# Optimization experiments

Hardware: AMD Instinct MI355X
Metric: run time of the kernel (lower is better)

The kernel has to match this reference:

```python
import jax, jax.numpy as jnp
import numpy as np

N = 50000      # nodes
E = 1600000    # edges (before self loops)
F_IN = 1433    # input features (Cora)
H1, C1 = 8, 8  # layer1: heads, out channels per head
C2 = 7         # layer2: classes (heads=1, concat=False)
SLOPE = 0.2    # PyG GATConv default negative_slope


def _gat_layer(x, src, dst, W, a_src, a_dst, b, heads, out_ch, concat):
    """PyG-style GATConv (eval mode, self loops already in src/dst)."""
    n = x.shape[0]
    h = (x @ W).reshape(n, heads, out_ch)                 # [N,H,C]
    alpha_s = jnp.einsum('nhc,hc->nh', h, a_src)          # [N,H]
    alpha_d = jnp.einsum('nhc,hc->nh', h, a_dst)          # [N,H]
    e = jax.nn.leaky_relu(alpha_s[src] + alpha_d[dst], SLOPE)  # [E,H]
    # segment softmax over incoming edges per destination node
    m = jax.ops.segment_max(e, dst, num_segments=n)       # [N,H]
    ex = jnp.exp(e - m[dst])
    denom = jax.ops.segment_sum(ex, dst, num_segments=n)  # [N,H]
    alpha = ex / (denom[dst] + 1e-16)                     # [E,H]
    out = jax.ops.segment_sum(h[src] * alpha[..., None], dst, num_segments=n)  # [N,H,C]
    out = out.reshape(n, heads * out_ch) if concat else out.mean(axis=1)
    return out + b


def setup_inputs() -> dict:
    key = jax.random.key(0)
    ks = jax.random.split(key, 10)
    x = jax.random.normal(ks[0], (N, F_IN), jnp.float32)
    edge_index = jax.random.randint(ks[1], (2, E), 0, N, jnp.int32)
    s = 0.1
    return {
        'x': x,
        'edge_index': edge_index,
        'W1': jax.random.normal(ks[2], (F_IN, H1 * C1), jnp.float32) * s,
        'att_src1': jax.random.normal(ks[3], (H1, C1), jnp.float32) * s,
        'att_dst1': jax.random.normal(ks[4], (H1, C1), jnp.float32) * s,
        'b1': jnp.zeros((H1 * C1,), jnp.float32),
        'W2': jax.random.normal(ks[5], (H1 * C1, C2), jnp.float32) * s,
        'att_src2': jax.random.normal(ks[6], (1, C2), jnp.float32) * s,
        'att_dst2': jax.random.normal(ks[7], (1, C2), jnp.float32) * s,
        'b2': jnp.zeros((C2,), jnp.float32),
    }


def reference(x, edge_index, W1, att_src1, att_dst1, b1, W2, att_src2, att_dst2, b2):
    loop = jnp.arange(N, dtype=edge_index.dtype)
    src = jnp.concatenate([edge_index[0], loop])   # add_self_loops=True
    dst = jnp.concatenate([edge_index[1], loop])
    h = _gat_layer(x, src, dst, W1, att_src1, att_dst1, b1, H1, C1, True)   # [N,64]
    h = jax.nn.elu(h)
    out = _gat_layer(h, src, dst, W2, att_src2, att_dst2, b2, 1, C2, False)  # [N,7]
    return jax.nn.log_softmax(out, axis=1)
```

## Files before the change

kernel.cpp:

```cpp
#include <hip/hip_runtime.h>
#include <hip/hip_bf16.h>

static constexpr int NN      = 50000;
static constexpr int FIN     = 1433;
static constexpr int KPAD    = 1440;
static constexpr int NB_SCAN = (NN + 255) / 256;
static constexpr int L1B     = NN / 4;

typedef __bf16 bf16x8 __attribute__((ext_vector_type(8)));
typedef float  f32x4  __attribute__((ext_vector_type(4)));

__device__ __forceinline__ float leaky02(float v){ return v >= 0.f ? v : 0.2f * v; }
__device__ __forceinline__ float bflo(unsigned u){ return __uint_as_float(u << 16); }
__device__ __forceinline__ float bfhi(unsigned u){ return __uint_as_float(u & 0xffff0000u); }

__device__ __forceinline__ void gld_lds4(const float* g, float* l){
    __builtin_amdgcn_global_load_lds(
        (const __attribute__((address_space(1))) unsigned int*)g,
        (__attribute__((address_space(3))) unsigned int*)l, 4, 0, 0);
}

__global__ __launch_bounds__(256) void k_prep(const float* __restrict__ W1,
                                              __bf16* __restrict__ w1h, __bf16* __restrict__ w1l,
                                              int* __restrict__ deg){
    int bid = blockIdx.x;
    if (bid < 64){
        int c = bid;
        for (int k = threadIdx.x; k < KPAD; k += 256){
            float v = (k < FIN) ? W1[(size_t)k * 64 + c] : 0.f;
            __bf16 hi = (__bf16)v;
            w1h[(size_t)c * KPAD + k] = hi;
            w1l[(size_t)c * KPAD + k] = (__bf16)(v - (float)hi);
        }
    } else {
        int i = (bid - 64) * 256 + threadIdx.x;
        if (i < NN) deg[i] = 0;
    }
}

__global__ __launch_bounds__(256) void k_rank(const int* __restrict__ dst, int* __restrict__ deg,
                                              int* __restrict__ rank, int E){
    int base = blockIdx.x * 1024 + threadIdx.x;
    int d[4]; bool v[4];
    #pragma unroll
    for (int i = 0; i < 4; ++i){
        int e = base + i * 256;
        v[i] = e < E;
        d[i] = v[i] ? dst[e] : 0;
    }
    int r[4];
    #pragma unroll
    for (int i = 0; i < 4; ++i)
        if (v[i]) r[i] = atomicAdd(&deg[d[i]], 1);
    #pragma unroll
    for (int i = 0; i < 4; ++i)
        if (v[i]) rank[base + i * 256] = r[i];
}

__global__ __launch_bounds__(256) void k_scan1(const int* __restrict__ deg, int* __restrict__ bsum){
    __shared__ int red[256];
    int i = blockIdx.x * 256 + threadIdx.x;
    red[threadIdx.x] = (i < NN) ? deg[i] : 0;
    __syncthreads();
    for (int off = 128; off > 0; off >>= 1){
        if (threadIdx.x < off) red[threadIdx.x] += red[threadIdx.x + off];
        __syncthreads();
    }
    if (threadIdx.x == 0) bsum[blockIdx.x] = red[0];
}

__global__ __launch_bounds__(256) void k_scan3(const int* __restrict__ deg, const int* __restrict__ bsum,
                                               int* __restrict__ row_off){
    __shared__ int s[256];
    int t = threadIdx.x;
    int i = blockIdx.x * 256 + t;
    s[t] = (t < blockIdx.x) ? bsum[t] : 0;
    __syncthreads();
    for (int off = 128; off > 0; off >>= 1){
        if (t < off) s[t] += s[t + off];
        __syncthreads();
    }
    int bofs = s[0];
    __syncthreads();
    int d = (i < NN) ? deg[i] : 0;
    s[t] = d;
    __syncthreads();
    for (int off = 1; off < 256; off <<= 1){
        int v = s[t];
        int a = (t >= off) ? s[t - off] : 0;
        __syncthreads();
        s[t] = v + a;
        __syncthreads();
    }
    int excl = s[t] - d + bofs;
    if (i < NN){
        row_off[i] = excl;
        if (i == NN - 1) row_off[NN] = excl + d;
    }
}

__global__ __launch_bounds__(256) void k_scatter(const int* __restrict__ src, const int* __restrict__ dst,
                                                 const int* __restrict__ rank, const int* __restrict__ row_off,
                                                 int* __restrict__ csr, int E){
    int base = blockIdx.x * 1024 + threadIdx.x;
    int d[4], r[4], sv[4]; bool v[4];
    #pragma unroll
    for (int i = 0; i < 4; ++i){
        int e = base + i * 256;
        v[i] = e < E;
        if (v[i]){ d[i] = dst[e]; r[i] = rank[e]; sv[i] = src[e]; }
    }
    int ro[4];
    #pragma unroll
    for (int i = 0; i < 4; ++i)
        if (v[i]) ro[i] = row_off[d[i]];
    #pragma unroll
    for (int i = 0; i < 4; ++i)
        if (v[i]) csr[ro[i] + r[i]] = sv[i];
}

__global__ __launch_bounds__(256, 4) void k_gemm1(const float* __restrict__ x,
    const __bf16* __restrict__ w1h, const __bf16* __restrict__ w1l,
    const float* __restrict__ a_s, const float* __restrict__ a_d,
    __bf16* __restrict__ Hb, __bf16* __restrict__ asad)
{
    __shared__ float  As[64 * 68];
    __shared__ __bf16 AH[64 * 72];
    __shared__ __bf16 AL[64 * 72];
    const int tid  = threadIdx.x;
    const int w    = tid >> 6;
    const int lane = tid & 63;
    const int lr   = lane & 15;
    const int lk   = lane >> 4;
    const int rbase = blockIdx.x * 64;
    const int cr = tid >> 2;
    const int cg = (tid & 3) * 16;

    unsigned rowoff[16];
    #pragma unroll
    for (int i = 0; i < 16; ++i){
        int rg = rbase + w * 16 + i; if (rg >= NN) rg = NN - 1;
        rowoff[i] = (unsigned)rg * (unsigned)FIN + (unsigned)lane;
    }

    const __bf16* bh_p = w1h + (size_t)(w * 16 + lr) * KPAD + lk * 8;
    const __bf16* bl_p = w1l + (size_t)(w * 16 + lr) * KPAD + lk * 8;

    f32x4 acc[4] = {{0,0,0,0},{0,0,0,0},{0,0,0,0},{0,0,0,0}};

    #pragma unroll
    for (int i = 0; i < 16; ++i)
        gld_lds4(x + rowoff[i], &As[(w * 16 + i) * 68]);
    __syncthreads();

    for (int kb = 0; kb < 22; ++kb){
        {
            const float* rp = &As[cr * 68 + cg];
            f32x4 v[4];
            #pragma unroll
            for (int j = 0; j < 4; ++j) v[j] = *(const f32x4*)(rp + j * 4);
            bf16x8 hv0, hv1, lv0, lv1;
            #pragma unroll
            for (int j = 0; j < 2; ++j){
                #pragma unroll
                for (int e = 0; e < 4; ++e){
                    float a0 = v[2 * j][e], a1 = v[2 * j + 1][e];
                    __bf16 h0 = (__bf16)a0, h1 = (__bf16)a1;
                    if (j == 0){ hv0[e] = h0; hv0[e + 4] = h1;
                                 lv0[e] = (__bf16)(a0 - (float)h0);
                                 lv0[e + 4] = (__bf16)(a1 - (float)h1); }
                    else       { hv1[e] = h0; hv1[e + 4] = h1;
                                 lv1[e] = (__bf16)(a0 - (float)h0);
                                 lv1[e + 4] = (__bf16)(a1 - (float)h1); }
                }
            }
            *(bf16x8*)&AH[cr * 72 + cg]     = hv0;
            *(bf16x8*)&AH[cr * 72 + cg + 8] = hv1;
            *(bf16x8*)&AL[cr * 72 + cg]     = lv0;
            *(bf16x8*)&AL[cr * 72 + cg + 8] = lv1;
        }
        __syncthreads();

        if (kb < 21){
            const float* gsrc = x + (kb + 1) * 64;
            #pragma unroll
            for (int i = 0; i < 16; ++i)
                gld_lds4(gsrc + rowoff[i], &As[(w * 16 + i) * 68]);
        }

        const int kA = kb * 64;
        bf16x8 bh0 = *(const bf16x8*)(bh_p + kA);
        bf16x8 bl0 = *(const bf16x8*)(bl_p + kA);
        bf16x8 bh1 = *(const bf16x8*)(bh_p + kA + 32);
        bf16x8 bl1 = *(const bf16x8*)(bl_p + kA + 32);
        #pragma unroll
        for (int ks = 0; ks < 2; ++ks){
            bf16x8 bh = ks ? bh1 : bh0;
            bf16x8 bl = ks ? bl1 : bl0;
            #pragma unroll
            for (int t = 0; t < 4; ++t){
                const int ao = (t * 16 + lr) * 72 + ks * 32 + lk * 8;
                bf16x8 ah = *(const bf16x8*)&AH[ao];
                bf16x8 al = *(const bf16x8*)&AL[ao];
                acc[t] = __builtin_amdgcn_mfma_f32_16x16x32_bf16(ah, bh, acc[t], 0, 0, 0);
                acc[t] = __builtin_amdgcn_mfma_f32_16x16x32_bf16(al, bh, acc[t], 0, 0, 0);
                acc[t] = __builtin_amdgcn_mfma_f32_16x16x32_bf16(ah, bl, acc[t], 0, 0, 0);
            }
        }
        __syncthreads();
    }

    {
        bf16x8 bh = *(const bf16x8*)(bh_p + 1408);
        bf16x8 bl = *(const bf16x8*)(bl_p + 1408);
        #pragma unroll
        for (int t = 0; t < 4; ++t){
            int rg = rbase + t * 16 + lr; if (rg >= NN) rg = NN - 1;
            const float* xr = x + (size_t)rg * FIN;
            bf16x8 ah, al;
            #pragma unroll
            for (int e = 0; e < 8; ++e){
                int k = 1408 + lk * 8 + e;
                float v = (k < FIN) ? xr[k] : 0.f;
                __bf16 h = (__bf16)v;
                ah[e] = h; al[e] = (__bf16)(v - (float)h);
            }
            acc[t] = __builtin_amdgcn_mfma_f32_16x16x32_bf16(ah, bh, acc[t], 0, 0, 0);
            acc[t] = __builtin_amdgcn_mfma_f32_16x16x32_bf16(al, bh, acc[t], 0, 0, 0);
            acc[t] = __builtin_amdgcn_mfma_f32_16x16x32_bf16(ah, bl, acc[t], 0, 0, 0);
        }
    }

    __syncthreads();
    const int col = w * 16 + lr;
    #pragma unroll
    for (int t = 0; t < 4; ++t){
        #pragma unroll
        for (int r = 0; r < 4; ++r){
            int rib = t * 16 + lk * 4 + r;
            float v = acc[t][r];
            As[rib * 68 + col] = v;
            int row = rbase + rib;
            if (row < NN) Hb[(size_t)row * 64 + col] = (__bf16)v;
        }
    }
    __syncthreads();
    #pragma unroll
    for (int it = 0; it < 2; ++it){
        int task = tid + it * 256;
        int row  = task >> 3;
        int hh   = task & 7;
        int grow = rbase + row;
        if (grow < NN){
            const float* hr = &As[row * 68 + hh * 8];
            float s = 0.f, dd = 0.f;
            #pragma unroll
            for (int c = 0; c < 8; ++c){
                float v = hr[c];
                s  = fmaf(v, a_s[hh * 8 + c], s);
                dd = fmaf(v, a_d[hh * 8 + c], dd);
            }
            asad[(size_t)grow * 16 + hh]     = (__bf16)s;
            asad[(size_t)grow * 16 + 8 + hh] = (__bf16)dd;
        }
    }
}

__global__ __launch_bounds__(256, 8) void k_layer1(const __bf16* __restrict__ asad,
    const __bf16* __restrict__ Hb, const int* __restrict__ row_off, const int* __restrict__ csr,
    const float* __restrict__ b1, float* __restrict__ x2)
{
    const int d  = blockIdx.x * 4 + (threadIdx.x >> 6);
    const int l  = threadIdx.x & 63;
    const int e8 = l >> 3;
    const int c8 = l & 7;
    const int c0 = c8 * 8;
    const float adv = (float)asad[(size_t)d * 16 + 8 + c8];

    float den = 0.f;
    float a[8] = {0.f,0.f,0.f,0.f,0.f,0.f,0.f,0.f};
    if (e8 == 0){
        float as_d = (float)asad[(size_t)d * 16 + c8];
        float p0 = __expf(leaky02(as_d + adv) - 20.f);
        uint4 hw = *(const uint4*)&Hb[(size_t)d * 64 + c0];
        den = p0;
        a[0] = p0 * bflo(hw.x); a[1] = p0 * bfhi(hw.x);
        a[2] = p0 * bflo(hw.y); a[3] = p0 * bfhi(hw.y);
        a[4] = p0 * bflo(hw.z); a[5] = p0 * bfhi(hw.z);
        a[6] = p0 * bflo(hw.w); a[7] = p0 * bfhi(hw.w);
    }

    const int beg = row_off[d], end = row_off[d + 1];
    const int nb = (end - beg + 7) >> 3;
    int csrv = 0;
    if (nb > 0){
        int idx = beg + c8; if (idx >= end) idx = end - 1;
        csrv = __builtin_nontemporal_load(csr + idx);
    }
    for (int b = 0; b < nb; ++b){
        const int base = beg + b * 8;
        int ncsr = 0;
        if (b + 1 < nb){
            int idx = base + 8 + c8; if (idx >= end) idx = end - 1;
            ncsr = __builtin_nontemporal_load(csr + idx);
        }
        int s = __shfl(csrv, e8, 8);
        const bool val = (base + e8) < end;
        uint4 hw = make_uint4(0u,0u,0u,0u); float av = 0.f;
        if (val){
            hw = *(const uint4*)&Hb[(size_t)s * 64 + c0];
            av = (float)asad[(size_t)s * 16 + c8];
        }
        if (val){
            float p = __expf(leaky02(av + adv) - 20.f);
            den += p;
            a[0] = fmaf(p, bflo(hw.x), a[0]); a[1] = fmaf(p, bfhi(hw.x), a[1]);
            a[2] = fmaf(p, bflo(hw.y), a[2]); a[3] = fmaf(p, bfhi(hw.y), a[3]);
            a[4] = fmaf(p, bflo(hw.z), a[4]); a[5] = fmaf(p, bfhi(hw.z), a[5]);
            a[6] = fmaf(p, bflo(hw.w), a[6]); a[7] = fmaf(p, bfhi(hw.w), a[7]);
        }
        csrv = ncsr;
    }

    #pragma unroll
    for (int m = 8; m <= 32; m <<= 1){
        den += __shfl_xor(den, m, 64);
        #pragma unroll
        for (int j = 0; j < 8; ++j) a[j] += __shfl_xor(a[j], m, 64);
    }

    if (e8 == 0){
        float inv = 1.f / den;
        float o[8];
        #pragma unroll
        for (int j = 0; j < 8; ++j){
            float v = a[j] * inv + b1[c0 + j];
            o[j] = (v > 0.f) ? v : (__expf(v) - 1.f);
        }
        float4 o0 = make_float4(o[0], o[1], o[2], o[3]);
        float4 o1 = make_float4(o[4], o[5], o[6], o[7]);
        float* xp = &x2[(size_t)d * 64 + c0];
        *(float4*)xp       = o0;
        *(float4*)(xp + 4) = o1;
    }
}

__global__ __launch_bounds__(256) void k_gemm2(const float* __restrict__ x2, const float* __restrict__ W2,
    const float* __restrict__ aw_in, const float* __restrict__ dw_in,
    float* __restrict__ h2a, float* __restrict__ ad2)
{
    __shared__ float w2s[448];
    __shared__ float aw[7], dw[7];
    int tid = threadIdx.x;
    for (int i = tid; i < 448; i += 256) w2s[i] = W2[i];
    if (tid < 7){ aw[tid] = aw_in[tid]; dw[tid] = dw_in[tid]; }
    __syncthreads();
    int n = blockIdx.x * 256 + tid;
    if (n >= NN) return;
    const float4* xp = (const float4*)(x2 + (size_t)n * 64);
    float acc[7] = {0.f,0.f,0.f,0.f,0.f,0.f,0.f};
    #pragma unroll
    for (int q = 0; q < 16; ++q){
        float4 v = xp[q];
        float vv[4] = {v.x, v.y, v.z, v.w};
        #pragma unroll
        for (int u = 0; u < 4; ++u){
            int k = q * 4 + u;
            #pragma unroll
            for (int c = 0; c < 7; ++c) acc[c] = fmaf(vv[u], w2s[k * 7 + c], acc[c]);
        }
    }
    float s = 0.f, d = 0.f;
    #pragma unroll
    for (int c = 0; c < 7; ++c){ s = fmaf(acc[c], aw[c], s); d = fmaf(acc[c], dw[c], d); }
    float* hp = h2a + (size_t)n * 8;
    #pragma unroll
    for (int c = 0; c < 7; ++c) hp[c] = acc[c];
    hp[7] = s;
    ad2[n] = d;
}

__global__ __launch_bounds__(256) void k_layer2(const float* __restrict__ ad2,
    const float* __restrict__ h2a, const int* __restrict__ row_off, const int* __restrict__ csr,
    const float* __restrict__ b2, float* __restrict__ out)
{
    int tid  = threadIdx.x;
    int node = blockIdx.x * 32 + (tid >> 3);
    int c    = tid & 7;
    int lane = tid & 63;
    int gb   = lane & ~7;
    if (node >= NN) return;
    float adv   = ad2[node];
    float vself = h2a[(size_t)node * 8 + c];
    float as_n  = __shfl(vself, gb + 7, 64);
    float e0 = leaky02(as_n + adv);
    float p0 = __expf(e0 - 20.f);
    float den = p0;
    float acc = p0 * vself;
    int beg = row_off[node], end = row_off[node + 1];
    for (int base = beg; base < end; base += 16){
        int cnt = end - base; if (cnt > 16) cnt = 16;
        int j1  = 8 + c;
        int cs0 = csr[base + (c  < cnt ? c  : cnt - 1)];
        int cs1 = csr[base + (j1 < cnt ? j1 : cnt - 1)];
        float val[16];
        #pragma unroll
        for (int t = 0; t < 16; ++t){
            if (t < cnt){
                int s = (t < 8) ? __shfl(cs0, gb + t, 64) : __shfl(cs1, gb + t - 8, 64);
                val[t] = h2a[(size_t)s * 8 + c];
            }
        }
        #pragma unroll
        for (int t = 0; t < 16; ++t){
            if (t < cnt){
                float as_s = __shfl(val[t], gb + 7, 64);
                float e = leaky02(as_s + adv);
                float p = __expf(e - 20.f);
                den += p;
                acc  = fmaf(p, val[t], acc);
            }
        }
    }
    float v = (c < 7) ? (acc / den + b2[c]) : -1e30f;
    float m = v;
    m = fmaxf(m, __shfl_xor(m, 1, 64));
    m = fmaxf(m, __shfl_xor(m, 2, 64));
    m = fmaxf(m, __shfl_xor(m, 4, 64));
    float ex = (c < 7) ? __expf(v - m) : 0.f;
    float s7 = ex;
    s7 += __shfl_xor(s7, 1, 64);
    s7 += __shfl_xor(s7, 2, 64);
    s7 += __shfl_xor(s7, 4, 64);
    if (c < 7) out[(size_t)node * 7 + c] = v - m - __logf(s7);
}

extern "C" void kernel_launch(void* const* d_in, const int* in_sizes, int n_in,
                              void* d_out, int out_size, void* d_ws, size_t ws_size,
                              hipStream_t stream)
{
    (void)n_in; (void)out_size; (void)ws_size;
    const float* x      = (const float*)d_in[0];
    const int*   ei     = (const int*)d_in[1];
    const int    E      = in_sizes[1] / 2;
    const float* W1     = (const float*)d_in[2];
    const float* asrc1  = (const float*)d_in[3];
    const float* adst1  = (const float*)d_in[4];
    const float* b1     = (const float*)d_in[5];
    const float* W2     = (const float*)d_in[6];
    const float* asrc2  = (const float*)d_in[7];
    const float* adst2  = (const float*)d_in[8];
    const float* b2     = (const float*)d_in[9];
    float* out = (float*)d_out;

    char* p = (char*)d_ws;
    auto alloc = [&](size_t bytes) -> void* {
        void* r = (void*)p;
        p += (bytes + 255) & ~(size_t)255;
        return r;
    };
    int*    deg     = (int*)alloc((size_t)NN * 4);
    int*    row_off = (int*)alloc((size_t)(NN + 1) * 4);
    int*    rank    = (int*)alloc((size_t)E * 4);
    int*    bsum    = (int*)alloc((size_t)NB_SCAN * 4);
    int*    csr     = (int*)alloc((size_t)E * 4);
    __bf16* w1h     = (__bf16*)alloc((size_t)64 * KPAD * 2);
    __bf16* w1l     = (__bf16*)alloc((size_t)64 * KPAD * 2);
    __bf16* Hb      = (__bf16*)alloc((size_t)NN * 64 * 2);
    __bf16* asad    = (__bf16*)alloc((size_t)NN * 16 * 2);
    float*  x2      = (float*)alloc((size_t)NN * 64 * 4);
    float*  h2a     = (float*)alloc((size_t)NN * 8 * 4);
    float*  ad2     = (float*)alloc((size_t)NN * 4);

    const int* src = ei;
    const int* dst = ei + E;

    k_prep   <<<64 + NB_SCAN, 256, 0, stream>>>(W1, w1h, w1l, deg);
    k_rank   <<<(E + 1023) / 1024, 256, 0, stream>>>(dst, deg, rank, E);
    k_scan1  <<<NB_SCAN, 256, 0, stream>>>(deg, bsum);
    k_scan3  <<<NB_SCAN, 256, 0, stream>>>(deg, bsum, row_off);
    k_scatter<<<(E + 1023) / 1024, 256, 0, stream>>>(src, dst, rank, row_off, csr, E);
    k_gemm1  <<<(NN + 63) / 64, 256, 0, stream>>>(x, w1h, w1l, asrc1, adst1, Hb, asad);
    k_layer1 <<<L1B, 256, 0, stream>>>(asad, Hb, row_off, csr, b1, x2);
    k_gemm2  <<<(NN + 255) / 256, 256, 0, stream>>>(x2, W2, asrc2, adst2, h2a, ad2);
    k_layer2 <<<(NN + 31) / 32, 256, 0, stream>>>(ad2, h2a, row_off, csr, b2, out);
}
```

Before: 298.3 us.

## Recompute attention logits from gathered features and compress layer-2 records to bf16

The per-node attention scores are no longer produced in the first GEMM and stored to a separate array. The layer-1 aggregation now recomputes the source and destination logits from the gathered bf16 feature rows, which removes one random gather per edge and the GEMM epilogue with its LDS round-trip. Layer 2 stores its per-node record (7 features plus source score) as 16-byte bf16 instead of 32-byte fp32. It also switches to one edge per lane with per-lane accumulation and a shuffle reduction, matching the layer-1 pattern. This trades extra FMAs per edge and some bf16 precision in layer 2 for less gather traffic.

```diff
diff --git a/kernel.cpp b/kernel.cpp
--- a/kernel.cpp
+++ b/kernel.cpp
@@ -121,8 +121,7 @@
 
 __global__ __launch_bounds__(256, 4) void k_gemm1(const float* __restrict__ x,
     const __bf16* __restrict__ w1h, const __bf16* __restrict__ w1l,
-    const float* __restrict__ a_s, const float* __restrict__ a_d,
-    __bf16* __restrict__ Hb, __bf16* __restrict__ asad)
+    __bf16* __restrict__ Hb)
 {
     __shared__ float  As[64 * 68];
     __shared__ __bf16 AH[64 * 72];
@@ -231,42 +230,19 @@
         }
     }
 
-    __syncthreads();
     const int col = w * 16 + lr;
     #pragma unroll
     for (int t = 0; t < 4; ++t){
         #pragma unroll
         for (int r = 0; r < 4; ++r){
-            int rib = t * 16 + lk * 4 + r;
-            float v = acc[t][r];
-            As[rib * 68 + col] = v;
-            int row = rbase + rib;
-            if (row < NN) Hb[(size_t)row * 64 + col] = (__bf16)v;
-        }
-    }
-    __syncthreads();
-    #pragma unroll
-    for (int it = 0; it < 2; ++it){
-        int task = tid + it * 256;
-        int row  = task >> 3;
-        int hh   = task & 7;
-        int grow = rbase + row;
-        if (grow < NN){
-            const float* hr = &As[row * 68 + hh * 8];
-            float s = 0.f, dd = 0.f;
-            #pragma unroll
-            for (int c = 0; c < 8; ++c){
-                float v = hr[c];
-                s  = fmaf(v, a_s[hh * 8 + c], s);
-                dd = fmaf(v, a_d[hh * 8 + c], dd);
-            }
-            asad[(size_t)grow * 16 + hh]     = (__bf16)s;
-            asad[(size_t)grow * 16 + 8 + hh] = (__bf16)dd;
-        }
-    }
-}
-
-__global__ __launch_bounds__(256, 8) void k_layer1(const __bf16* __restrict__ asad,
+            int row = rbase + t * 16 + lk * 4 + r;
+            if (row < NN) Hb[(size_t)row * 64 + col] = (__bf16)acc[t][r];
+        }
+    }
+}
+
+__global__ __launch_bounds__(256, 8) void k_layer1(const float* __restrict__ a_s,
+    const float* __restrict__ a_d,
     const __bf16* __restrict__ Hb, const int* __restrict__ row_off, const int* __restrict__ csr,
     const float* __restrict__ b1, float* __restrict__ x2)
 {
@@ -275,19 +251,31 @@
     const int e8 = l >> 3;
     const int c8 = l & 7;
     const int c0 = c8 * 8;
-    const float adv = (float)asad[(size_t)d * 16 + 8 + c8];
+
+    float asw[8], adw[8];
+    #pragma unroll
+    for (int j = 0; j < 8; ++j){ asw[j] = a_s[c0 + j]; adw[j] = a_d[c0 + j]; }
 
     float den = 0.f;
     float a[8] = {0.f,0.f,0.f,0.f,0.f,0.f,0.f,0.f};
-    if (e8 == 0){
-        float as_d = (float)asad[(size_t)d * 16 + c8];
-        float p0 = __expf(leaky02(as_d + adv) - 20.f);
-        uint4 hw = *(const uint4*)&Hb[(size_t)d * 64 + c0];
-        den = p0;
-        a[0] = p0 * bflo(hw.x); a[1] = p0 * bfhi(hw.x);
-        a[2] = p0 * bflo(hw.y); a[3] = p0 * bfhi(hw.y);
-        a[4] = p0 * bflo(hw.z); a[5] = p0 * bfhi(hw.z);
-        a[6] = p0 * bflo(hw.w); a[7] = p0 * bfhi(hw.w);
+    float adv;
+    {
+        uint4 hs = *(const uint4*)&Hb[(size_t)d * 64 + c0];
+        float hv[8] = { bflo(hs.x), bfhi(hs.x), bflo(hs.y), bfhi(hs.y),
+                        bflo(hs.z), bfhi(hs.z), bflo(hs.w), bfhi(hs.w) };
+        float ad_ = 0.f, as_ = 0.f;
+        #pragma unroll
+        for (int j = 0; j < 8; ++j){
+            ad_ = fmaf(hv[j], adw[j], ad_);
+            as_ = fmaf(hv[j], asw[j], as_);
+        }
+        adv = ad_;
+        if (e8 == 0){
+            float p0 = __expf(leaky02(as_ + adv) - 20.f);
+            den = p0;
+            #pragma unroll
+            for (int j = 0; j < 8; ++j) a[j] = p0 * hv[j];
+        }
     }
 
     const int beg = row_off[d], end = row_off[d + 1];
@@ -306,18 +294,18 @@
         }
         int s = __shfl(csrv, e8, 8);
         const bool val = (base + e8) < end;
-        uint4 hw = make_uint4(0u,0u,0u,0u); float av = 0.f;
+        uint4 hw = make_uint4(0u,0u,0u,0u);
+        if (val) hw = *(const uint4*)&Hb[(size_t)s * 64 + c0];
         if (val){
-            hw = *(const uint4*)&Hb[(size_t)s * 64 + c0];
-            av = (float)asad[(size_t)s * 16 + c8];
-        }
-        if (val){
+            float g[8] = { bflo(hw.x), bfhi(hw.x), bflo(hw.y), bfhi(hw.y),
+                           bflo(hw.z), bfhi(hw.z), bflo(hw.w), bfhi(hw.w) };
+            float av = 0.f;
+            #pragma unroll
+            for (int j = 0; j < 8; ++j) av = fmaf(g[j], asw[j], av);
             float p = __expf(leaky02(av + adv) - 20.f);
             den += p;
-            a[0] = fmaf(p, bflo(hw.x), a[0]); a[1] = fmaf(p, bfhi(hw.x), a[1]);
-            a[2] = fmaf(p, bflo(hw.y), a[2]); a[3] = fmaf(p, bfhi(hw.y), a[3]);
-            a[4] = fmaf(p, bflo(hw.z), a[4]); a[5] = fmaf(p, bfhi(hw.z), a[5]);
-            a[6] = fmaf(p, bflo(hw.w), a[6]); a[7] = fmaf(p, bfhi(hw.w), a[7]);
+            #pragma unroll
+            for (int j = 0; j < 8; ++j) a[j] = fmaf(p, g[j], a[j]);
         }
         csrv = ncsr;
     }
@@ -337,17 +325,15 @@
             float v = a[j] * inv + b1[c0 + j];
             o[j] = (v > 0.f) ? v : (__expf(v) - 1.f);
         }
-        float4 o0 = make_float4(o[0], o[1], o[2], o[3]);
-        float4 o1 = make_float4(o[4], o[5], o[6], o[7]);
         float* xp = &x2[(size_t)d * 64 + c0];
-        *(float4*)xp       = o0;
-        *(float4*)(xp + 4) = o1;
+        *(float4*)xp       = make_float4(o[0], o[1], o[2], o[3]);
+        *(float4*)(xp + 4) = make_float4(o[4], o[5], o[6], o[7]);
     }
 }
 
 __global__ __launch_bounds__(256) void k_gemm2(const float* __restrict__ x2, const float* __restrict__ W2,
     const float* __restrict__ aw_in, const float* __restrict__ dw_in,
-    float* __restrict__ h2a, float* __restrict__ ad2)
+    __bf16* __restrict__ h2b, float* __restrict__ ad2)
 {
     __shared__ float w2s[448];
     __shared__ float aw[7], dw[7];
@@ -373,66 +359,89 @@
     float s = 0.f, d = 0.f;
     #pragma unroll
     for (int c = 0; c < 7; ++c){ s = fmaf(acc[c], aw[c], s); d = fmaf(acc[c], dw[c], d); }
-    float* hp = h2a + (size_t)n * 8;
-    #pragma unroll
-    for (int c = 0; c < 7; ++c) hp[c] = acc[c];
-    hp[7] = s;
+    __bf16 rec[8];
+    #pragma unroll
+    for (int c = 0; c < 7; ++c) rec[c] = (__bf16)acc[c];
+    rec[7] = (__bf16)s;
+    *(uint4*)&h2b[(size_t)n * 8] = *(uint4*)rec;
     ad2[n] = d;
 }
 
-__global__ __launch_bounds__(256) void k_layer2(const float* __restrict__ ad2,
-    const float* __restrict__ h2a, const int* __restrict__ row_off, const int* __restrict__ csr,
+__global__ __launch_bounds__(256, 8) void k_layer2(const float* __restrict__ ad2,
+    const __bf16* __restrict__ h2b, const int* __restrict__ row_off, const int* __restrict__ csr,
     const float* __restrict__ b2, float* __restrict__ out)
 {
     int tid  = threadIdx.x;
     int node = blockIdx.x * 32 + (tid >> 3);
-    int c    = tid & 7;
-    int lane = tid & 63;
-    int gb   = lane & ~7;
+    int sl   = tid & 7;
     if (node >= NN) return;
-    float adv   = ad2[node];
-    float vself = h2a[(size_t)node * 8 + c];
-    float as_n  = __shfl(vself, gb + 7, 64);
-    float e0 = leaky02(as_n + adv);
-    float p0 = __expf(e0 - 20.f);
-    float den = p0;
-    float acc = p0 * vself;
-    int beg = row_off[node], end = row_off[node + 1];
-    for (int base = beg; base < end; base += 16){
-        int cnt = end - base; if (cnt > 16) cnt = 16;
-        int j1  = 8 + c;
-        int cs0 = csr[base + (c  < cnt ? c  : cnt - 1)];
-        int cs1 = csr[base + (j1 < cnt ? j1 : cnt - 1)];
-        float val[16];
-        #pragma unroll
-        for (int t = 0; t < 16; ++t){
-            if (t < cnt){
-                int s = (t < 8) ? __shfl(cs0, gb + t, 64) : __shfl(cs1, gb + t - 8, 64);
-                val[t] = h2a[(size_t)s * 8 + c];
-            }
-        }
-        #pragma unroll
-        for (int t = 0; t < 16; ++t){
-            if (t < cnt){
-                float as_s = __shfl(val[t], gb + 7, 64);
-                float e = leaky02(as_s + adv);
-                float p = __expf(e - 20.f);
-                den += p;
-                acc  = fmaf(p, val[t], acc);
-            }
-        }
-    }
-    float v = (c < 7) ? (acc / den + b2[c]) : -1e30f;
-    float m = v;
-    m = fmaxf(m, __shfl_xor(m, 1, 64));
-    m = fmaxf(m, __shfl_xor(m, 2, 64));
-    m = fmaxf(m, __shfl_xor(m, 4, 64));
-    float ex = (c < 7) ? __expf(v - m) : 0.f;
-    float s7 = ex;
-    s7 += __shfl_xor(s7, 1, 64);
-    s7 += __shfl_xor(s7, 2, 64);
-    s7 += __shfl_xor(s7, 4, 64);
-    if (c < 7) out[(size_t)node * 7 + c] = v - m - __logf(s7);
+    float adv = ad2[node];
+
+    float den = 0.f;
+    float a[7] = {0.f,0.f,0.f,0.f,0.f,0.f,0.f};
+    {
+        uint4 hs = *(const uint4*)&h2b[(size_t)node * 8];
+        float h[8] = { bflo(hs.x), bfhi(hs.x), bflo(hs.y), bfhi(hs.y),
+                       bflo(hs.z), bfhi(hs.z), bflo(hs.w), bfhi(hs.w) };
+        if (sl == 0){
+            float p0 = __expf(leaky02(h[7] + adv) - 20.f);
+            den = p0;
+            #pragma unroll
+            for (int c = 0; c < 7; ++c) a[c] = p0 * h[c];
+        }
+    }
+
+    const int beg = row_off[node], end = row_off[node + 1];
+    const int nb = (end - beg + 7) >> 3;
+    int csrv = 0;
+    if (nb > 0){
+        int idx = beg + sl; if (idx >= end) idx = end - 1;
+        csrv = __builtin_nontemporal_load(csr + idx);
+    }
+    for (int b = 0; b < nb; ++b){
+        const int base = beg + b * 8;
+        int ncsr = 0;
+        if (b + 1 < nb){
+            int idx = base + 8 + sl; if (idx >= end) idx = end - 1;
+            ncsr = __builtin_nontemporal_load(csr + idx);
+        }
+        const bool val = (base + sl) < end;
+        uint4 hw = make_uint4(0u,0u,0u,0u);
+        if (val) hw = *(const uint4*)&h2b[(size_t)csrv * 8];
+        if (val){
+            float g[8] = { bflo(hw.x), bfhi(hw.x), bflo(hw.y), bfhi(hw.y),
+                           bflo(hw.z), bfhi(hw.z), bflo(hw.w), bfhi(hw.w) };
+            float p = __expf(leaky02(g[7] + adv) - 20.f);
+            den += p;
+            #pragma unroll
+            for (int c = 0; c < 7; ++c) a[c] = fmaf(p, g[c], a[c]);
+        }
+        csrv = ncsr;
+    }
+
+    #pragma unroll
+    for (int m = 1; m <= 4; m <<= 1){
+        den += __shfl_xor(den, m, 64);
+        #pragma unroll
+        for (int c = 0; c < 7; ++c) a[c] += __shfl_xor(a[c], m, 64);
+    }
+
+    if (sl == 0){
+        float inv = 1.f / den;
+        float v[7];
+        #pragma unroll
+        for (int c = 0; c < 7; ++c) v[c] = a[c] * inv + b2[c];
+        float mx = v[0];
+        #pragma unroll
+        for (int c = 1; c < 7; ++c) mx = fmaxf(mx, v[c]);
+        float s7 = 0.f;
+        #pragma unroll
+        for (int c = 0; c < 7; ++c) s7 += __expf(v[c] - mx);
+        float lg = mx + __logf(s7);
+        float* op = &out[(size_t)node * 7];
+        #pragma unroll
+        for (int c = 0; c < 7; ++c) op[c] = v[c] - lg;
+    }
 }
 
 extern "C" void kernel_launch(void* const* d_in, const int* in_sizes, int n_in,
@@ -467,9 +476,8 @@
     __bf16* w1h     = (__bf16*)alloc((size_t)64 * KPAD * 2);
     __bf16* w1l     = (__bf16*)alloc((size_t)64 * KPAD * 2);
     __bf16* Hb      = (__bf16*)alloc((size_t)NN * 64 * 2);
-    __bf16* asad    = (__bf16*)alloc((size_t)NN * 16 * 2);
     float*  x2      = (float*)alloc((size_t)NN * 64 * 4);
-    float*  h2a     = (float*)alloc((size_t)NN * 8 * 4);
+    __bf16* h2b     = (__bf16*)alloc((size_t)NN * 8 * 2);
     float*  ad2     = (float*)alloc((size_t)NN * 4);
 
     const int* src = ei;
@@ -480,8 +488,8 @@
     k_scan1  <<<NB_SCAN, 256, 0, stream>>>(deg, bsum);
     k_scan3  <<<NB_SCAN, 256, 0, stream>>>(deg, bsum, row_off);
     k_scatter<<<(E + 1023) / 1024, 256, 0, stream>>>(src, dst, rank, row_off, csr, E);
-    k_gemm1  <<<(NN + 63) / 64, 256, 0, stream>>>(x, w1h, w1l, asrc1, adst1, Hb, asad);
-    k_layer1 <<<L1B, 256, 0, stream>>>(asad, Hb, row_off, csr, b1, x2);
-    k_gemm2  <<<(NN + 255) / 256, 256, 0, stream>>>(x2, W2, asrc2, adst2, h2a, ad2);
-    k_layer2 <<<(NN + 31) / 32, 256, 0, stream>>>(ad2, h2a, row_off, csr, b2, out);
-}
+    k_gemm1  <<<(NN + 63) / 64, 256, 0, stream>>>(x, w1h, w1l, Hb);
+    k_layer1 <<<L1B, 256, 0, stream>>>(asrc1, adst1, Hb, row_off, csr, b1, x2);
+    k_gemm2  <<<(NN + 255) / 256, 256, 0, stream>>>(x2, W2, asrc2, adst2, h2b, ad2);
+    k_layer2 <<<(NN + 31) / 32, 256, 0, stream>>>(ad2, h2b, row_off, csr, b2, out);
+}
```

New measurement: 289.8 us. -2.8%, faster.
